# Performance work log

Hardware: AMD Instinct MI355X
Metric: run time of the kernel (lower is better)

Reference implementation:

```python
import jax, jax.numpy as jnp
import numpy as np

N = 100000      # nodes
E = 1600000     # edges (avg degree 16)
DIN = 32        # input feature dim
H = 16          # nhidden
DEPTH = 4       # number of SAGEConv layers


def setup_inputs() -> dict:
    key = jax.random.key(0)
    ks = jax.random.split(key, 16)
    s = 0.1
    inp = {
        "x": jax.random.normal(ks[0], (N, DIN), jnp.float32),
        "edge_index": jax.random.randint(ks[1], (2, E), 0, N, dtype=jnp.int64),
        # SAGEConv layer 0: in=DIN -> out=H. lin_l has bias, lin_r has no bias (PyG default).
        "Wl0": jax.random.normal(ks[2], (H, DIN), jnp.float32) * s,
        "bl0": jnp.zeros((H,), jnp.float32),
        "Wr0": jax.random.normal(ks[3], (H, DIN), jnp.float32) * s,
        # SAGEConv layers 1..3: in=H -> out=H, stacked.
        "Wls": jax.random.normal(ks[4], (DEPTH - 1, H, H), jnp.float32) * s,
        "bls": jnp.zeros((DEPTH - 1, H), jnp.float32),
        "Wrs": jax.random.normal(ks[5], (DEPTH - 1, H, H), jnp.float32) * s,
        # lin_out MLP: [H, 2H, 2H, 1] with acts [silu, silu, None], no batch norm.
        "W1": jax.random.normal(ks[6], (2 * H, H), jnp.float32) * s,
        "b1": jnp.zeros((2 * H,), jnp.float32),
        "W2": jax.random.normal(ks[7], (2 * H, 2 * H), jnp.float32) * s,
        "b2": jnp.zeros((2 * H,), jnp.float32),
        "W3": jax.random.normal(ks[8], (1, 2 * H), jnp.float32) * s,
        "b3": jnp.zeros((1,), jnp.float32),
    }
    return inp


def reference(x, edge_index, Wl0, bl0, Wr0, Wls, bls, Wrs, W1, b1, W2, b2, W3, b3):
    src = edge_index[0]  # message source (x_j)
    dst = edge_index[1]  # aggregation target (x_i)

    def sage(h, Wl, bl, Wr):
        # sum-aggregate neighbor features, then lin_l(agg) + lin_r(h)
        agg = jax.ops.segment_sum(h[src], dst, num_segments=N)  # [N, d]
        return agg @ Wl.T + bl + h @ Wr.T

    x = jax.nn.silu(sage(x, Wl0, bl0, Wr0))
    for i in range(DEPTH - 1):
        x = jax.nn.silu(sage(x, Wls[i], bls[i], Wrs[i]))

    out = jax.nn.silu(x @ W1.T + b1)
    out = jax.nn.silu(out @ W2.T + b2)
    out = out @ W3.T + b3  # [N, 1]
    return out
```

## Files before the change

kernel.cpp:

```cpp
#include <hip/hip_runtime.h>


#define SH      8
#define BWID    256
#define NBK     512
#define CHUNK   2048
#define EPT     (CHUNK / 256)
#define BCAP    5120

__device__ __forceinline__ float silu_f(float v) {
    return v * __builtin_amdgcn_rcpf(1.0f + __expf(-v));
}

__device__ __forceinline__ float bf_lo(unsigned u) { return __uint_as_float(u << 16); }
__device__ __forceinline__ float bf_hi(unsigned u) { return __uint_as_float(u & 0xFFFF0000u); }
__device__ __forceinline__ unsigned short f2bf(float f) {
    unsigned x = __float_as_uint(f);
    unsigned r = x + 0x7FFFu + ((x >> 16) & 1u);
    return (unsigned short)(r >> 16);
}
__device__ __forceinline__ unsigned pack_bf2(float a, float b) {
    return (unsigned)f2bf(a) | ((unsigned)f2bf(b) << 16);
}

#define ACC2(u0, u1) \
    p[0] += bf_lo(u0.x); p[1] += bf_hi(u0.x); p[2] += bf_lo(u0.y); p[3] += bf_hi(u0.y); \
    p[4] += bf_lo(u0.z); p[5] += bf_hi(u0.z); p[6] += bf_lo(u0.w); p[7] += bf_hi(u0.w); \
    p[8] += bf_lo(u1.x); p[9] += bf_hi(u1.x); p[10]+= bf_lo(u1.y); p[11]+= bf_hi(u1.y); \
    p[12]+= bf_lo(u1.z); p[13]+= bf_hi(u1.z); p[14]+= bf_lo(u1.w); p[15]+= bf_hi(u1.w);


__global__ __launch_bounds__(256) void bin_dense0(
    const int* __restrict__ src, const int* __restrict__ dst,
    unsigned short* __restrict__ cnt16,
    unsigned short* __restrict__ scan16,
    unsigned* __restrict__ binned0,
    const float* __restrict__ x,
    const float* __restrict__ Wl0, const float* __restrict__ bl0,
    const float* __restrict__ Wr0,
    unsigned* __restrict__ hlb, float* __restrict__ acc,
    int n, int ne, int nblocks)
{
    __shared__ int      s_hist[NBK];
    __shared__ int      s_off[NBK];
    __shared__ int      s_p[256];
    __shared__ unsigned s_items[CHUNK];
    __shared__ float    sWl[512], sWr[512], sbl[16];

    const int t = threadIdx.x;
    const int blk = blockIdx.x;
    for (int i = t; i < 512; i += 256) { sWl[i] = Wl0[i]; sWr[i] = Wr0[i]; }
    if (t < 16) sbl[t] = bl0[t];

    const int base = blk * CHUNK;
    const int cnt = min(CHUNK, ne - base);

    int es[EPT], ed[EPT];
#pragma unroll
    for (int j = 0; j < EPT; ++j) {
        const int i = t + j * 256;
        if (i < cnt) { es[j] = src[base + i]; ed[j] = dst[base + i]; }
        else         { es[j] = -1; ed[j] = -1; }
    }

    s_hist[t] = 0; s_hist[t + 256] = 0;
    __syncthreads();
#pragma unroll
    for (int j = 0; j < EPT; ++j)
        if (es[j] >= 0) atomicAdd(&s_hist[ed[j] >> SH], 1);
    __syncthreads();

    const int c0 = s_hist[2 * t], c1 = s_hist[2 * t + 1];
    const int ps = c0 + c1;
    s_p[t] = ps;
    __syncthreads();
    int v = ps;
    for (int o = 1; o < 256; o <<= 1) {
        const int add = (t >= o) ? s_p[t - o] : 0;
        __syncthreads();
        v += add;
        s_p[t] = v;
        __syncthreads();
    }
    const int ex = v - ps;
    s_off[2 * t] = ex;
    s_off[2 * t + 1] = ex + c0;

    cnt16[blk * NBK + t]        = (unsigned short)s_hist[t];
    cnt16[blk * NBK + t + 256]  = (unsigned short)s_hist[t + 256];
    s_hist[t] = 0; s_hist[t + 256] = 0;
    __syncthreads();
    scan16[blk * NBK + t]       = (unsigned short)s_off[t];
    scan16[blk * NBK + t + 256] = (unsigned short)s_off[t + 256];

#pragma unroll
    for (int j = 0; j < EPT; ++j) {
        if (es[j] >= 0) {
            const int b  = ed[j] >> SH;
            const int ld = ed[j] & (BWID - 1);
            const int r  = atomicAdd(&s_hist[b], 1);
            s_items[s_off[b] + r] = ((unsigned)ld << 17) | (unsigned)es[j];
        }
    }
    __syncthreads();

    for (int i = t; i < cnt; i += 256)
        binned0[base + i] = s_items[i];

    if (t >= 128) return;
    const int node = blk * 128 + t;
    if (node >= n) return;

    float h[32];
    const float4* __restrict__ xp = (const float4*)(x + (size_t)node * 32);
#pragma unroll
    for (int r = 0; r < 8; ++r) {
        const float4 vv = xp[r];
        h[4*r+0] = vv.x; h[4*r+1] = vv.y; h[4*r+2] = vv.z; h[4*r+3] = vv.w;
    }

    const float4* __restrict__ sWl4 = (const float4*)sWl;
    const float4* __restrict__ sWr4 = (const float4*)sWr;
    float ol[16], oa[16];
#pragma unroll
    for (int j = 0; j < 16; ++j) {
        float al = 0.f, ar = 0.f;
#pragma unroll
        for (int d4 = 0; d4 < 8; ++d4) {
            const float4 wl = sWl4[j * 8 + d4];
            const float4 wr = sWr4[j * 8 + d4];
            al = fmaf(wl.x, h[4*d4+0], al); al = fmaf(wl.y, h[4*d4+1], al);
            al = fmaf(wl.z, h[4*d4+2], al); al = fmaf(wl.w, h[4*d4+3], al);
            ar = fmaf(wr.x, h[4*d4+0], ar); ar = fmaf(wr.y, h[4*d4+1], ar);
            ar = fmaf(wr.z, h[4*d4+2], ar); ar = fmaf(wr.w, h[4*d4+3], ar);
        }
        ol[j] = al;
        oa[j] = sbl[j] + ar;
    }

    unsigned u[8];
#pragma unroll
    for (int r = 0; r < 8; ++r) u[r] = pack_bf2(ol[2*r], ol[2*r+1]);
    uint4* __restrict__ hp = (uint4*)(hlb + (size_t)node * 8);
    hp[0] = make_uint4(u[0], u[1], u[2], u[3]);
    hp[1] = make_uint4(u[4], u[5], u[6], u[7]);
    float4* __restrict__ ap = (float4*)(acc + (size_t)node * 16);
#pragma unroll
    for (int r = 0; r < 4; ++r)
        ap[r] = make_float4(oa[4*r], oa[4*r+1], oa[4*r+2], oa[4*r+3]);
}

__global__ __launch_bounds__(512) void node_sort(
    const unsigned* __restrict__ binned0,
    const unsigned short* __restrict__ cnt16,
    const unsigned short* __restrict__ scan16,
    int* __restrict__ binned1,
    int2* __restrict__ noff2,
    int n, int nblocks)
{
    __shared__ unsigned s_edges[BCAP];
    __shared__ int cnt[BWID];
    __shared__ int off_[BWID];
    __shared__ int s_p[512];
    __shared__ int s_tot;
    const int b = blockIdx.x, t = threadIdx.x;
    const int dbase = b * BCAP;

    int rc[4], rs[4];
    int myc = 0;
#pragma unroll
    for (int j = 0; j < 4; ++j) {
        const int i = 4 * t + j;
        if (i < nblocks) { rc[j] = cnt16[i * NBK + b]; rs[j] = scan16[i * NBK + b]; }
        else             { rc[j] = 0; rs[j] = 0; }
        myc += rc[j];
    }
    s_p[t] = myc;
    __syncthreads();
    int v = myc;
    for (int o = 1; o < 512; o <<= 1) {
        const int add = (t >= o) ? s_p[t - o] : 0;
        __syncthreads();
        v += add;
        s_p[t] = v;
        __syncthreads();
    }
    int o = v - myc;
    if (t == 511) s_tot = v;
    if (t < BWID) cnt[t] = 0;

#pragma unroll
    for (int j = 0; j < 4; ++j) {
        if (rc[j]) {
            const unsigned* __restrict__ run =
                binned0 + (size_t)(4 * t + j) * CHUNK + rs[j];
            for (int r = 0; r < rc[j]; ++r) s_edges[o++] = run[r];
        }
    }
    __syncthreads();
    const int tot = s_tot;

    for (int k = t; k < tot; k += 512)
        atomicAdd(&cnt[s_edges[k] >> 17], 1);
    __syncthreads();

    if (t < BWID) off_[t] = cnt[t];
    __syncthreads();
    for (int o2 = 1; o2 < BWID; o2 <<= 1) {
        const int add = (t < BWID && t >= o2) ? off_[t - o2] : 0;
        __syncthreads();
        if (t < BWID) off_[t] += add;
        __syncthreads();
    }
    if (t < BWID) off_[t] -= cnt[t];
    __syncthreads();

    if (t < BWID) {
        const int node = (b << SH) + t;
        if (node < n)
            noff2[node] = make_int2(dbase + off_[t], dbase + off_[t] + cnt[t]);
        cnt[t] = 0;
    }
    __syncthreads();

    for (int k = t; k < tot; k += 512) {
        const unsigned u = s_edges[k];
        const int ld = (int)(u >> 17);
        const int r2 = atomicAdd(&cnt[ld], 1);
        binned1[dbase + off_[ld] + r2] = (int)(u & 0x1FFFFu);
    }
}


__device__ __forceinline__ void gather16_4(
    const int* __restrict__ binned1, const uint4* __restrict__ h4,
    int beg, int end, int q, float* p)
{
#pragma unroll
    for (int i = 0; i < 16; ++i) p[i] = 0.f;
    int base = beg;
    for (; base + 16 <= end; base += 16) {
        const int k = base + q * 4;
        const int i0 = binned1[k],     i1 = binned1[k + 1];
        const int i2 = binned1[k + 2], i3 = binned1[k + 3];
        const uint4 a0 = h4[(size_t)i0 * 2], a1 = h4[(size_t)i0 * 2 + 1];
        const uint4 b0 = h4[(size_t)i1 * 2], b1 = h4[(size_t)i1 * 2 + 1];
        const uint4 c0 = h4[(size_t)i2 * 2], c1 = h4[(size_t)i2 * 2 + 1];
        const uint4 d0 = h4[(size_t)i3 * 2], d1 = h4[(size_t)i3 * 2 + 1];
        ACC2(a0, a1)
        ACC2(b0, b1)
        ACC2(c0, c1)
        ACC2(d0, d1)
    }
    for (int k = base + q; k < end; k += 4) {
        const int s0 = binned1[k];
        const uint4 a0 = h4[(size_t)s0 * 2], a1 = h4[(size_t)s0 * 2 + 1];
        ACC2(a0, a1)
    }
#pragma unroll
    for (int i = 0; i < 16; ++i) p[i] += __shfl_xor(p[i], 1);
#pragma unroll
    for (int i = 0; i < 16; ++i) p[i] += __shfl_xor(p[i], 2);
}

__global__ __launch_bounds__(256, 4) void fused_agg_dense(
    const int2* __restrict__ noff2, const int* __restrict__ binned1,
    const unsigned* __restrict__ hl_in, const float* __restrict__ acc_in,
    const float* __restrict__ Wl, const float* __restrict__ bl,
    const float* __restrict__ Wr,
    unsigned* __restrict__ hl_out, float* __restrict__ acc_out, int n)
{
    __shared__ float sWl[256], sWr[256], sbl[16];
    const int t = threadIdx.x;
    sWl[t] = Wl[t]; sWr[t] = Wr[t];
    if (t < 16) sbl[t] = bl[t];
    __syncthreads();

    const int gid = blockIdx.x * 256 + t;
    const int node = gid >> 2;
    if (node >= n) return;
    const int q = t & 3;
    const int2 be = noff2[node];

    float p[16];
    gather16_4(binned1, (const uint4*)hl_in, be.x, be.y, q, p);

    const float4* __restrict__ ai = (const float4*)(acc_in + (size_t)node * 16);
    float h[16];
#pragma unroll
    for (int r = 0; r < 4; ++r) {
        const float4 a = ai[r];
        h[4*r+0] = silu_f(a.x + p[4*r+0]);
        h[4*r+1] = silu_f(a.y + p[4*r+1]);
        h[4*r+2] = silu_f(a.z + p[4*r+2]);
        h[4*r+3] = silu_f(a.w + p[4*r+3]);
    }

    const float4* __restrict__ sWl4 = (const float4*)sWl;
    const float4* __restrict__ sWr4 = (const float4*)sWr;
    float ol[4], oa[4];
#pragma unroll
    for (int jj = 0; jj < 4; ++jj) {
        const int j = 4 * q + jj;
        float al = 0.f, ar = 0.f;
#pragma unroll
        for (int d4 = 0; d4 < 4; ++d4) {
            const float4 wl = sWl4[j * 4 + d4];
            const float4 wr = sWr4[j * 4 + d4];
            al = fmaf(wl.x, h[4*d4+0], al); al = fmaf(wl.y, h[4*d4+1], al);
            al = fmaf(wl.z, h[4*d4+2], al); al = fmaf(wl.w, h[4*d4+3], al);
            ar = fmaf(wr.x, h[4*d4+0], ar); ar = fmaf(wr.y, h[4*d4+1], ar);
            ar = fmaf(wr.z, h[4*d4+2], ar); ar = fmaf(wr.w, h[4*d4+3], ar);
        }
        ol[jj] = al;
        oa[jj] = sbl[j] + ar;
    }

    ((uint2*)hl_out)[(size_t)node * 4 + q] =
        make_uint2(pack_bf2(ol[0], ol[1]), pack_bf2(ol[2], ol[3]));
    ((float4*)acc_out)[(size_t)node * 4 + q] =
        make_float4(oa[0], oa[1], oa[2], oa[3]);
}

__global__ __launch_bounds__(256, 3) void fused_agg_mlp(
    const int2* __restrict__ noff2, const int* __restrict__ binned1,
    const unsigned* __restrict__ hl_in, const float* __restrict__ acc_in,
    const float* __restrict__ W1, const float* __restrict__ b1,
    const float* __restrict__ W2, const float* __restrict__ b2,
    const float* __restrict__ W3, const float* __restrict__ b3,
    float* __restrict__ out, int n)
{
    __shared__ float sW1[512], sW2[1024], sb1[32], sb2[32], sW3[32];
    __shared__ float sb3;
    const int t = threadIdx.x;
    for (int i = t; i < 512; i += 256) sW1[i] = W1[i];
    for (int i = t; i < 1024; i += 256) sW2[i] = W2[i];
    if (t < 32) { sb1[t] = b1[t]; sb2[t] = b2[t]; sW3[t] = W3[t]; }
    if (t == 0) sb3 = b3[0];
    __syncthreads();

    const int gid = blockIdx.x * 256 + t;
    const int node = gid >> 2;
    if (node >= n) return;
    const int q = t & 3;
    const int2 be = noff2[node];

    float p[16];
    gather16_4(binned1, (const uint4*)hl_in, be.x, be.y, q, p);

    const float4* __restrict__ ai = (const float4*)(acc_in + (size_t)node * 16);
    float h[16];
#pragma unroll
    for (int r = 0; r < 4; ++r) {
        const float4 a = ai[r];
        h[4*r+0] = silu_f(a.x + p[4*r+0]);
        h[4*r+1] = silu_f(a.y + p[4*r+1]);
        h[4*r+2] = silu_f(a.z + p[4*r+2]);
        h[4*r+3] = silu_f(a.w + p[4*r+3]);
    }

    const float4* __restrict__ sW1v = (const float4*)sW1;
    float a1[8];
#pragma unroll
    for (int jj = 0; jj < 8; ++jj) {
        const int j = 8 * q + jj;
        float s = sb1[j];
#pragma unroll
        for (int d4 = 0; d4 < 4; ++d4) {
            const float4 w = sW1v[j * 4 + d4];
            s = fmaf(w.x, h[4*d4+0], s); s = fmaf(w.y, h[4*d4+1], s);
            s = fmaf(w.z, h[4*d4+2], s); s = fmaf(w.w, h[4*d4+3], s);
        }
        a1[jj] = silu_f(s);
    }

    float t0[16];
#pragma unroll
    for (int i = 0; i < 8; ++i) {
        const float mine  = a1[i];
        const float other = __shfl_xor(mine, 1);
        const bool hi = (q & 1);
        t0[i]     = hi ? other : mine;
        t0[8 + i] = hi ? mine  : other;
    }
    float A1[32];
#pragma unroll
    for (int i = 0; i < 16; ++i) {
        const float mine  = t0[i];
        const float other = __shfl_xor(mine, 2);
        const bool hi = (q & 2);
        A1[i]      = hi ? other : mine;
        A1[16 + i] = hi ? mine  : other;
    }

    const float4* __restrict__ sW2v = (const float4*)sW2;
    float part = 0.f;
#pragma unroll
    for (int jj = 0; jj < 8; ++jj) {
        const int j = 8 * q + jj;
        float s = sb2[j];
#pragma unroll
        for (int d4 = 0; d4 < 8; ++d4) {
            const float4 w = sW2v[j * 8 + d4];
            s = fmaf(w.x, A1[4*d4+0], s); s = fmaf(w.y, A1[4*d4+1], s);
            s = fmaf(w.z, A1[4*d4+2], s); s = fmaf(w.w, A1[4*d4+3], s);
        }
        part = fmaf(sW3[j], silu_f(s), part);
    }
    part += __shfl_xor(part, 1);
    part += __shfl_xor(part, 2);
    if (q == 0) out[node] = part + sb3;
}

extern "C" void kernel_launch(void* const* d_in, const int* in_sizes, int n_in,
                              void* d_out, int out_size, void* d_ws, size_t ws_size,
                              hipStream_t stream)
{
    const float* x   = (const float*)d_in[0];
    const int*   ei  = (const int*)d_in[1];
    const float* Wl0 = (const float*)d_in[2];
    const float* bl0 = (const float*)d_in[3];
    const float* Wr0 = (const float*)d_in[4];
    const float* Wls = (const float*)d_in[5];
    const float* bls = (const float*)d_in[6];
    const float* Wrs = (const float*)d_in[7];
    const float* W1  = (const float*)d_in[8];
    const float* b1  = (const float*)d_in[9];
    const float* W2  = (const float*)d_in[10];
    const float* b2  = (const float*)d_in[11];
    const float* W3  = (const float*)d_in[12];
    const float* b3  = (const float*)d_in[13];

    const int n  = in_sizes[0] / 32;
    const int ne = in_sizes[1] / 2;
    const int* src = ei;
    const int* dst = ei + ne;
    const int nbuck   = (n + BWID - 1) >> SH;
    const int nblocks = (ne + CHUNK - 1) / CHUNK;

    float*    acc0    = (float*)d_ws;
    float*    acc1    = acc0 + (size_t)n * 16;
    unsigned* hlbA    = (unsigned*)(acc1 + (size_t)n * 16);
    unsigned* hlbB    = hlbA + (size_t)n * 8;
    int2*     noff2   = (int2*)(hlbB + (size_t)n * 8);
    int*      binned1 = (int*)(noff2 + n);
    unsigned short* cnt16  = (unsigned short*)(binned1 + (size_t)nbuck * BCAP);
    unsigned short* scan16 = cnt16 + (size_t)nblocks * NBK;
    unsigned* binned0 = (unsigned*)(scan16 + (size_t)nblocks * NBK);

    const int lb = (n * 4 + 255) / 256;

    bin_dense0<<<nblocks, 256, 0, stream>>>(src, dst, cnt16, scan16, binned0,
                                            x, Wl0, bl0, Wr0, hlbA, acc0,
                                            n, ne, nblocks);
    node_sort<<<nbuck, 512, 0, stream>>>(binned0, cnt16, scan16, binned1, noff2,
                                         n, nblocks);

    fused_agg_dense<<<lb, 256, 0, stream>>>(noff2, binned1, hlbA, acc0,
        Wls + 0,   bls + 0,  Wrs + 0,   hlbB, acc1, n);
    fused_agg_dense<<<lb, 256, 0, stream>>>(noff2, binned1, hlbB, acc1,
        Wls + 256, bls + 16, Wrs + 256, hlbA, acc0, n);
    fused_agg_dense<<<lb, 256, 0, stream>>>(noff2, binned1, hlbA, acc0,
        Wls + 512, bls + 32, Wrs + 512, hlbB, acc1, n);
    fused_agg_mlp<<<lb, 256, 0, stream>>>(noff2, binned1, hlbB, acc1,
        W1, b1, W2, b2, W3, b3, (float*)d_out, n);
}
```

Measured before the change: 155.8 us.

## Fuse node sort with first aggregation layer into one kernel

```diff
diff --git a/kernel.cpp b/kernel.cpp
--- a/kernel.cpp
+++ b/kernel.cpp
@@ -150,87 +150,35 @@
         ap[r] = make_float4(oa[4*r], oa[4*r+1], oa[4*r+2], oa[4*r+3]);
 }
 
-__global__ __launch_bounds__(512) void node_sort(
-    const unsigned* __restrict__ binned0,
-    const unsigned short* __restrict__ cnt16,
-    const unsigned short* __restrict__ scan16,
-    int* __restrict__ binned1,
-    int2* __restrict__ noff2,
-    int n, int nblocks)
-{
-    __shared__ unsigned s_edges[BCAP];
-    __shared__ int cnt[BWID];
-    __shared__ int off_[BWID];
-    __shared__ int s_p[512];
-    __shared__ int s_tot;
-    const int b = blockIdx.x, t = threadIdx.x;
-    const int dbase = b * BCAP;
-
-    int rc[4], rs[4];
-    int myc = 0;
-#pragma unroll
-    for (int j = 0; j < 4; ++j) {
-        const int i = 4 * t + j;
-        if (i < nblocks) { rc[j] = cnt16[i * NBK + b]; rs[j] = scan16[i * NBK + b]; }
-        else             { rc[j] = 0; rs[j] = 0; }
-        myc += rc[j];
-    }
-    s_p[t] = myc;
-    __syncthreads();
-    int v = myc;
-    for (int o = 1; o < 512; o <<= 1) {
-        const int add = (t >= o) ? s_p[t - o] : 0;
-        __syncthreads();
-        v += add;
-        s_p[t] = v;
-        __syncthreads();
-    }
-    int o = v - myc;
-    if (t == 511) s_tot = v;
-    if (t < BWID) cnt[t] = 0;
-
-#pragma unroll
-    for (int j = 0; j < 4; ++j) {
-        if (rc[j]) {
-            const unsigned* __restrict__ run =
-                binned0 + (size_t)(4 * t + j) * CHUNK + rs[j];
-            for (int r = 0; r < rc[j]; ++r) s_edges[o++] = run[r];
-        }
-    }
-    __syncthreads();
-    const int tot = s_tot;
-
-    for (int k = t; k < tot; k += 512)
-        atomicAdd(&cnt[s_edges[k] >> 17], 1);
-    __syncthreads();
-
-    if (t < BWID) off_[t] = cnt[t];
-    __syncthreads();
-    for (int o2 = 1; o2 < BWID; o2 <<= 1) {
-        const int add = (t < BWID && t >= o2) ? off_[t - o2] : 0;
-        __syncthreads();
-        if (t < BWID) off_[t] += add;
-        __syncthreads();
-    }
-    if (t < BWID) off_[t] -= cnt[t];
-    __syncthreads();
-
-    if (t < BWID) {
-        const int node = (b << SH) + t;
-        if (node < n)
-            noff2[node] = make_int2(dbase + off_[t], dbase + off_[t] + cnt[t]);
-        cnt[t] = 0;
-    }
-    __syncthreads();
-
-    for (int k = t; k < tot; k += 512) {
-        const unsigned u = s_edges[k];
-        const int ld = (int)(u >> 17);
-        const int r2 = atomicAdd(&cnt[ld], 1);
-        binned1[dbase + off_[ld] + r2] = (int)(u & 0x1FFFFu);
-    }
-}
-
+
+__device__ __forceinline__ void gather16_2(
+    const int* __restrict__ binned1, const uint4* __restrict__ h4,
+    int beg, int end, int q, float* p)
+{
+#pragma unroll
+    for (int i = 0; i < 16; ++i) p[i] = 0.f;
+    int base = beg;
+    for (; base + 8 <= end; base += 8) {
+        const int k = base + q * 4;
+        const int i0 = binned1[k],     i1 = binned1[k + 1];
+        const int i2 = binned1[k + 2], i3 = binned1[k + 3];
+        const uint4 a0 = h4[(size_t)i0 * 2], a1 = h4[(size_t)i0 * 2 + 1];
+        const uint4 b0 = h4[(size_t)i1 * 2], b1 = h4[(size_t)i1 * 2 + 1];
+        const uint4 c0 = h4[(size_t)i2 * 2], c1 = h4[(size_t)i2 * 2 + 1];
+        const uint4 d0 = h4[(size_t)i3 * 2], d1 = h4[(size_t)i3 * 2 + 1];
+        ACC2(a0, a1)
+        ACC2(b0, b1)
+        ACC2(c0, c1)
+        ACC2(d0, d1)
+    }
+    for (int k = base + q; k < end; k += 2) {
+        const int s0 = binned1[k];
+        const uint4 a0 = h4[(size_t)s0 * 2], a1 = h4[(size_t)s0 * 2 + 1];
+        ACC2(a0, a1)
+    }
+#pragma unroll
+    for (int i = 0; i < 16; ++i) p[i] += __shfl_xor(p[i], 1);
+}
 
 __device__ __forceinline__ void gather16_4(
     const int* __restrict__ binned1, const uint4* __restrict__ h4,
@@ -263,6 +211,145 @@
     for (int i = 0; i < 16; ++i) p[i] += __shfl_xor(p[i], 2);
 }
 
+__global__ __launch_bounds__(512, 4) void sort_agg_dense(
+    const unsigned* __restrict__ binned0,
+    const unsigned short* __restrict__ cnt16,
+    const unsigned short* __restrict__ scan16,
+    int* __restrict__ binned1,
+    int2* __restrict__ noff2,
+    const unsigned* __restrict__ hl_in,
+    const float* __restrict__ acc_in,
+    const float* __restrict__ Wl, const float* __restrict__ bl,
+    const float* __restrict__ Wr,
+    unsigned* __restrict__ hl_out, float* __restrict__ acc_out,
+    int n, int nblocks)
+{
+    __shared__ unsigned s_edges[BCAP];
+    __shared__ int cnt[BWID];
+    __shared__ int off_[BWID];
+    __shared__ int s_p[512];
+    __shared__ int s_tot;
+    __shared__ float sWl[256], sWr[256], sbl[16];
+    const int b = blockIdx.x, t = threadIdx.x;
+    const int dbase = b * BCAP;
+
+    if (t < 256) { sWl[t] = Wl[t]; sWr[t] = Wr[t]; }
+    if (t < 16) sbl[t] = bl[t];
+
+    int rc[4], rs[4];
+    int myc = 0;
+#pragma unroll
+    for (int j = 0; j < 4; ++j) {
+        const int i = 4 * t + j;
+        if (i < nblocks) { rc[j] = cnt16[i * NBK + b]; rs[j] = scan16[i * NBK + b]; }
+        else             { rc[j] = 0; rs[j] = 0; }
+        myc += rc[j];
+    }
+    s_p[t] = myc;
+    __syncthreads();
+    int v = myc;
+    for (int o = 1; o < 512; o <<= 1) {
+        const int add = (t >= o) ? s_p[t - o] : 0;
+        __syncthreads();
+        v += add;
+        s_p[t] = v;
+        __syncthreads();
+    }
+    int o = v - myc;
+    if (t == 511) s_tot = v;
+    if (t < BWID) cnt[t] = 0;
+
+#pragma unroll
+    for (int j = 0; j < 4; ++j) {
+        if (rc[j]) {
+            const unsigned* __restrict__ run =
+                binned0 + (size_t)(4 * t + j) * CHUNK + rs[j];
+            for (int r = 0; r < rc[j]; ++r) s_edges[o++] = run[r];
+        }
+    }
+    __syncthreads();
+    const int tot = s_tot;
+
+    for (int k = t; k < tot; k += 512)
+        atomicAdd(&cnt[s_edges[k] >> 17], 1);
+    __syncthreads();
+
+    if (t < BWID) off_[t] = cnt[t];
+    __syncthreads();
+    for (int o2 = 1; o2 < BWID; o2 <<= 1) {
+        const int add = (t < BWID && t >= o2) ? off_[t - o2] : 0;
+        __syncthreads();
+        if (t < BWID) off_[t] += add;
+        __syncthreads();
+    }
+    if (t < BWID) off_[t] -= cnt[t];
+    __syncthreads();
+
+    if (t < BWID) {
+        const int node = (b << SH) + t;
+        if (node < n)
+            noff2[node] = make_int2(dbase + off_[t], dbase + off_[t] + cnt[t]);
+        cnt[t] = 0;
+    }
+    __syncthreads();
+
+    for (int k = t; k < tot; k += 512) {
+        const unsigned u = s_edges[k];
+        const int ld = (int)(u >> 17);
+        const int r2 = atomicAdd(&cnt[ld], 1);
+        binned1[dbase + off_[ld] + r2] = (int)(u & 0x1FFFFu);
+    }
+    __syncthreads();
+
+    const int ln = t >> 1;
+    const int node = (b << SH) + ln;
+    if (node >= n) return;
+    const int q = t & 1;
+    const int beg = dbase + off_[ln];
+    const int end = beg + cnt[ln];
+
+    float p[16];
+    gather16_2(binned1, (const uint4*)hl_in, beg, end, q, p);
+
+    const float4* __restrict__ ai = (const float4*)(acc_in + (size_t)node * 16);
+    float h[16];
+#pragma unroll
+    for (int r = 0; r < 4; ++r) {
+        const float4 a = ai[r];
+        h[4*r+0] = silu_f(a.x + p[4*r+0]);
+        h[4*r+1] = silu_f(a.y + p[4*r+1]);
+        h[4*r+2] = silu_f(a.z + p[4*r+2]);
+        h[4*r+3] = silu_f(a.w + p[4*r+3]);
+    }
+
+    const float4* __restrict__ sWl4 = (const float4*)sWl;
+    const float4* __restrict__ sWr4 = (const float4*)sWr;
+    float ol[8], oa[8];
+#pragma unroll
+    for (int jj = 0; jj < 8; ++jj) {
+        const int j = 8 * q + jj;
+        float al = 0.f, ar = 0.f;
+#pragma unroll
+        for (int d4 = 0; d4 < 4; ++d4) {
+            const float4 wl = sWl4[j * 4 + d4];
+            const float4 wr = sWr4[j * 4 + d4];
+            al = fmaf(wl.x, h[4*d4+0], al); al = fmaf(wl.y, h[4*d4+1], al);
+            al = fmaf(wl.z, h[4*d4+2], al); al = fmaf(wl.w, h[4*d4+3], al);
+            ar = fmaf(wr.x, h[4*d4+0], ar); ar = fmaf(wr.y, h[4*d4+1], ar);
+            ar = fmaf(wr.z, h[4*d4+2], ar); ar = fmaf(wr.w, h[4*d4+3], ar);
+        }
+        ol[jj] = al;
+        oa[jj] = sbl[j] + ar;
+    }
+
+    ((uint4*)hl_out)[(size_t)node * 2 + q] =
+        make_uint4(pack_bf2(ol[0], ol[1]), pack_bf2(ol[2], ol[3]),
+                   pack_bf2(ol[4], ol[5]), pack_bf2(ol[6], ol[7]));
+    float4* __restrict__ ap = (float4*)(acc_out + (size_t)node * 16);
+    ap[2 * q]     = make_float4(oa[0], oa[1], oa[2], oa[3]);
+    ap[2 * q + 1] = make_float4(oa[4], oa[5], oa[6], oa[7]);
+}
+
 __global__ __launch_bounds__(256, 4) void fused_agg_dense(
     const int2* __restrict__ noff2, const int* __restrict__ binned1,
     const unsigned* __restrict__ hl_in, const float* __restrict__ acc_in,
@@ -453,11 +540,10 @@
     bin_dense0<<<nblocks, 256, 0, stream>>>(src, dst, cnt16, scan16, binned0,
                                             x, Wl0, bl0, Wr0, hlbA, acc0,
                                             n, ne, nblocks);
-    node_sort<<<nbuck, 512, 0, stream>>>(binned0, cnt16, scan16, binned1, noff2,
-                                         n, nblocks);
-
-    fused_agg_dense<<<lb, 256, 0, stream>>>(noff2, binned1, hlbA, acc0,
-        Wls + 0,   bls + 0,  Wrs + 0,   hlbB, acc1, n);
+    sort_agg_dense<<<nbuck, 512, 0, stream>>>(binned0, cnt16, scan16,
+        binned1, noff2, hlbA, acc0,
+        Wls + 0, bls + 0, Wrs + 0, hlbB, acc1, n, nblocks);
+
     fused_agg_dense<<<lb, 256, 0, stream>>>(noff2, binned1, hlbB, acc1,
         Wls + 256, bls + 16, Wrs + 256, hlbA, acc0, n);
     fused_agg_dense<<<lb, 256, 0, stream>>>(noff2, binned1, hlbA, acc0,
```

Result: faster. 151.2 us (-2.9%).
